# Kernel optimization log

Hardware: AMD Instinct MI355X
Metric: run time of the kernel (lower is better)

The kernel has to match this reference:

```python
import jax, jax.numpy as jnp
import numpy as np

H = 6      # n_attention_heads
BLK = 64


def adder1x1(x2d, w):
    """AdderNet 1x1 'convolution': Y[co, n] = -sum_ci |x2d[ci, n] - w[co, ci]|.
    Processed in output-channel blocks to bound the abs-diff intermediate.
    x2d: [Ci, N], w: [Co, Ci] -> [Co, N]
    """
    co, ci = w.shape
    wb = w.reshape(co // BLK, BLK, ci)
    def f(wblk):  # wblk: [BLK, Ci] -> [BLK, N]
        return -jnp.sum(jnp.abs(x2d[None, :, :] - wblk[:, :, None]), axis=1)
    return jax.lax.map(f, wb).reshape(co, -1)


def layernorm_all(y, w, b, eps=1e-5):
    # nn.LayerNorm([E, B, S]) applied to [1, E, B, S]: normalize over ALL of E,B,S
    mu = jnp.mean(y)
    var = jnp.mean((y - mu) ** 2)
    return (y - mu) * jax.lax.rsqrt(var + eps) * w + b


def layernorm_last(y, w, b, eps=1e-5):
    mu = jnp.mean(y, axis=-1, keepdims=True)
    var = jnp.mean((y - mu) ** 2, axis=-1, keepdims=True)
    return (y - mu) * jax.lax.rsqrt(var + eps) * w + b


def setup_inputs() -> dict:
    key = jax.random.key(0)
    ks = jax.random.split(key, 14)
    B, S, E = 8, 197, 384
    inp = {
        "x": jax.random.normal(ks[0], (B, S, E), jnp.float32),
        "wq": jax.random.normal(ks[1], (E, E), jnp.float32) * 0.05,
        "wk": jax.random.normal(ks[2], (E, E), jnp.float32) * 0.05,
        "wv": jax.random.normal(ks[3], (E, E), jnp.float32) * 0.05,
        "qln_w": 1.0 + 0.02 * jax.random.normal(ks[4], (E, B, S), jnp.float32),
        "qln_b": 0.02 * jax.random.normal(ks[5], (E, B, S), jnp.float32),
        "kln_w": 1.0 + 0.02 * jax.random.normal(ks[6], (E, B, S), jnp.float32),
        "kln_b": 0.02 * jax.random.normal(ks[7], (E, B, S), jnp.float32),
        "vln_w": 1.0 + 0.02 * jax.random.normal(ks[8], (E, B, S), jnp.float32),
        "vln_b": 0.02 * jax.random.normal(ks[9], (E, B, S), jnp.float32),
        "oln_w": 1.0 + 0.02 * jax.random.normal(ks[10], (E,), jnp.float32),
        "oln_b": 0.02 * jax.random.normal(ks[11], (E,), jnp.float32),
        "fc_w": jax.random.normal(ks[12], (E, E), jnp.float32) * 0.05,
        "fc_b": 0.02 * jax.random.normal(ks[13], (E,), jnp.float32),
    }
    return inp


def reference(x, wq, wk, wv, qln_w, qln_b, kln_w, kln_b, vln_w, vln_b,
              oln_w, oln_b, fc_w, fc_b):
    B, S, E = x.shape
    D = E // H
    scale = (2.0 * D * (1.0 - 2.0 / np.pi)) ** (-0.5)

    # torch: x.reshape(1, E, B, S) on contiguous [B,S,E] is a flat-buffer reshape
    x2d = x.reshape(E, B * S)  # [Ci, N]

    def proj(w, lw, lb):
        y = adder1x1(x2d, w).reshape(E, B, S)          # adder2d 1x1, bias=False
        y = layernorm_all(y, lw, lb)                    # LN over [E,B,S]
        y = y.reshape(B, S, H, D)                       # flat reshape (as torch)
        y = jnp.swapaxes(y, 1, 2)                       # [B,H,S,D]
        return y.reshape(B * H, S, D)

    q = proj(wq, qln_w, qln_b)
    k = proj(wk, kln_w, kln_b)
    v = proj(wv, vln_w, vln_b)

    att = jnp.einsum('bsd,btd->bst', q, k) * scale      # [B*H, S, S]
    att = jax.nn.softmax(att, axis=-1) + jnp.eye(S, dtype=x.dtype)
    o = jnp.einsum('bst,btd->bsd', att, v)              # [B*H, S, D]

    o = jnp.swapaxes(o.reshape(B, H, S, D), 1, 2).reshape(B, S, E)
    o = layernorm_last(o, oln_w, oln_b)
    return o @ fc_w.T + fc_b
```

## Files before the change

### kernel.cpp

```cpp
#include <hip/hip_runtime.h>
#include <math.h>

#ifndef M_PI
#define M_PI 3.14159265358979323846
#endif

#define B_ 8
#define S_ 197
#define E_ 384
#define H_ 6
#define D_ 64
#define N_ (B_*S_)
#define EN ((size_t)E_*N_)
#define NBLK_RED 591

__global__ __launch_bounds__(256) void k_adder(
    const float* __restrict__ x,
    const float* __restrict__ wq, const float* __restrict__ wk,
    const float* __restrict__ wv,
    float* __restrict__ P)
{
  const int z = blockIdx.z;
  const int p = z >> 1, c = z & 1;
  const float* __restrict__ w = (p == 0) ? wq : (p == 1) ? wk : wv;
  const int co0 = blockIdx.x * 64;
  const int n0  = blockIdx.y * 32;
  const int cib = c * 192;

  __shared__ float Xs[16][32];
  __shared__ float Ws[16][64];

  const int tid = threadIdx.x;
  const int tx = tid & 15;
  const int ty = tid >> 4;

  const int xr = tid >> 4, xc = (tid & 15) * 2;
  const int wr = tid >> 2, wc = (tid & 3) * 4;

  const bool xok = (n0 + xc + 1) < N_;
  const float* xg = x + (size_t)(cib + xr) * N_ + n0 + xc;
  const float* wg = w + (size_t)(co0 + wr) * E_ + cib + wc;

  float2 xv = xok ? *(const float2*)xg : make_float2(0.f, 0.f);
  float4 wv4 = *(const float4*)wg;

  float acc[4][2];
  #pragma unroll
  for (int i = 0; i < 4; ++i) { acc[i][0] = 0.f; acc[i][1] = 0.f; }

  #pragma unroll 1
  for (int t = 0; t < 12; ++t) {
    if (t > 0) __syncthreads();
    *(float2*)(&Xs[xr][xc]) = xv;
    Ws[wc + 0][wr] = wv4.x; Ws[wc + 1][wr] = wv4.y;
    Ws[wc + 2][wr] = wv4.z; Ws[wc + 3][wr] = wv4.w;
    __syncthreads();
    if (t < 11) {
      xg += (size_t)16 * N_;
      wg += 16;
      xv = xok ? *(const float2*)xg : make_float2(0.f, 0.f);
      wv4 = *(const float4*)wg;
    }
    #pragma unroll
    for (int cc = 0; cc < 16; ++cc) {
      float2 x2 = *(const float2*)(&Xs[cc][tx * 2]);
      float4 w4 = *(const float4*)(&Ws[cc][ty * 4]);
      float xa[2] = {x2.x, x2.y};
      float wa[4] = {w4.x, w4.y, w4.z, w4.w};
      #pragma unroll
      for (int i = 0; i < 4; ++i)
        #pragma unroll
        for (int j = 0; j < 2; ++j)
          acc[i][j] += fabsf(xa[j] - wa[i]);
    }
  }

  const int nb = n0 + tx * 2;
  if (nb + 1 < N_) {
    #pragma unroll
    for (int i = 0; i < 4; ++i) {
      int co = co0 + ty * 4 + i;
      float2 yv; yv.x = acc[i][0]; yv.y = acc[i][1];
      *(float2*)(P + (size_t)z * EN + (size_t)co * N_ + nb) = yv;
    }
  }
}

__global__ __launch_bounds__(256) void k_reduceY(
    float* __restrict__ wsbuf, float* __restrict__ partials)
{
  const int p = blockIdx.y;
  float* P0 = wsbuf + (size_t)(2 * p) * EN;
  const float* P1 = wsbuf + (size_t)(2 * p + 1) * EN;
  const int tid = threadIdx.x;
  size_t i = ((size_t)blockIdx.x * 256 + tid) * 4;
  float4 a = *(const float4*)(P0 + i);
  float4 b = *(const float4*)(P1 + i);
  float4 y;
  y.x = -(a.x + b.x); y.y = -(a.y + b.y);
  y.z = -(a.z + b.z); y.w = -(a.w + b.w);
  *(float4*)(P0 + i) = y;
  float s1 = y.x + y.y + y.z + y.w;
  float s2 = y.x * y.x + y.y * y.y + y.z * y.z + y.w * y.w;
  #pragma unroll
  for (int off = 32; off > 0; off >>= 1) {
    s1 += __shfl_down(s1, off);
    s2 += __shfl_down(s2, off);
  }
  __shared__ float red[8];
  int wid = tid >> 6, lane = tid & 63;
  if (lane == 0) { red[wid * 2] = s1; red[wid * 2 + 1] = s2; }
  __syncthreads();
  if (tid == 0) {
    float t1 = red[0] + red[2] + red[4] + red[6];
    float t2 = red[1] + red[3] + red[5] + red[7];
    partials[((size_t)p * NBLK_RED + blockIdx.x) * 2 + 0] = t1;
    partials[((size_t)p * NBLK_RED + blockIdx.x) * 2 + 1] = t2;
  }
}

__global__ __launch_bounds__(256) void k_stats(
    const float* __restrict__ partials, float* __restrict__ stats)
{
  const int p = blockIdx.x;
  const int tid = threadIdx.x;
  float s1 = 0.f, s2 = 0.f;
  for (int i = tid; i < NBLK_RED; i += 256) {
    s1 += partials[((size_t)p * NBLK_RED + i) * 2 + 0];
    s2 += partials[((size_t)p * NBLK_RED + i) * 2 + 1];
  }
  #pragma unroll
  for (int off = 32; off > 0; off >>= 1) {
    s1 += __shfl_down(s1, off);
    s2 += __shfl_down(s2, off);
  }
  __shared__ float red[8];
  int wid = tid >> 6, lane = tid & 63;
  if (lane == 0) { red[wid * 2] = s1; red[wid * 2 + 1] = s2; }
  __syncthreads();
  if (tid == 0) {
    float S1 = red[0] + red[2] + red[4] + red[6];
    float S2 = red[1] + red[3] + red[5] + red[7];
    float mean = S1 / (float)EN;
    float var = S2 / (float)EN - mean * mean;
    stats[p * 2 + 0] = mean;
    stats[p * 2 + 1] = rsqrtf(var + 1e-5f);
  }
}

__global__ __launch_bounds__(256) void k_lnall(
    float* __restrict__ wsbuf, const float* __restrict__ stats,
    const float* __restrict__ w0, const float* __restrict__ b0,
    const float* __restrict__ w1, const float* __restrict__ b1,
    const float* __restrict__ w2, const float* __restrict__ b2)
{
  const int p = blockIdx.y;
  const float* __restrict__ w = (p == 0) ? w0 : (p == 1) ? w1 : w2;
  const float* __restrict__ b = (p == 0) ? b0 : (p == 1) ? b1 : b2;
  const float mean = stats[p * 2 + 0];
  const float rstd = stats[p * 2 + 1];
  size_t i = ((size_t)blockIdx.x * 256 + threadIdx.x) * 4;
  const float* Yp = wsbuf + (size_t)(2 * p) * EN;
  float* Zp = wsbuf + (size_t)(2 * p + 1) * EN;
  float4 y = *(const float4*)(Yp + i);
  float4 wv = *(const float4*)(w + i);
  float4 bv = *(const float4*)(b + i);
  float4 z;
  z.x = (y.x - mean) * rstd * wv.x + bv.x;
  z.y = (y.y - mean) * rstd * wv.y + bv.y;
  z.z = (y.z - mean) * rstd * wv.z + bv.z;
  z.w = (y.w - mean) * rstd * wv.w + bv.w;
  *(float4*)(Zp + i) = z;
}

__global__ __launch_bounds__(256) void k_attn(
    const float* __restrict__ zq, const float* __restrict__ zk,
    const float* __restrict__ zv, float* __restrict__ obuf, float scale)
{
  const int bh = blockIdx.x, b = bh / H_, h = bh % H_;
  const int s0 = blockIdx.y * 32;

  __shared__ float Qs[64][36];
  __shared__ float KVs[64][68];
  __shared__ float Ps[32][200];
  __shared__ float linv[32];

  const int tid = threadIdx.x;
  const int tx = tid & 15, ty = tid >> 4;

  #pragma unroll
  for (int it = 0; it < 2; ++it) {
    int idx = tid + it * 256;
    int sl = idx >> 4, c4 = (idx & 15) * 4;
    int s = s0 + sl;
    float4 v = make_float4(0.f, 0.f, 0.f, 0.f);
    if (s < S_) v = *(const float4*)(zq + (size_t)(b * S_ + s) * E_ + h * D_ + c4);
    Qs[c4 + 0][sl] = v.x; Qs[c4 + 1][sl] = v.y;
    Qs[c4 + 2][sl] = v.z; Qs[c4 + 3][sl] = v.w;
  }

  float accS[4][2][4];
  #pragma unroll
  for (int tt = 0; tt < 4; ++tt)
    #pragma unroll
    for (int r = 0; r < 2; ++r)
      #pragma unroll
      for (int j = 0; j < 4; ++j) accS[tt][r][j] = 0.f;

  #pragma unroll
  for (int tt = 0; tt < 4; ++tt) {
    __syncthreads();
    #pragma unroll
    for (int it = 0; it < 4; ++it) {
      int idx = tid + it * 256;
      int tl = idx >> 4, c4 = (idx & 15) * 4;
      int t = tt * 64 + tl;
      float4 u = make_float4(0.f, 0.f, 0.f, 0.f);
      if (t < S_) u = *(const float4*)(zk + (size_t)(b * S_ + t) * E_ + h * D_ + c4);
      KVs[c4 + 0][tl] = u.x; KVs[c4 + 1][tl] = u.y;
      KVs[c4 + 2][tl] = u.z; KVs[c4 + 3][tl] = u.w;
    }
    __syncthreads();
    #pragma unroll 8
    for (int d = 0; d < 64; ++d) {
      float2 q2 = *(const float2*)(&Qs[d][2 * ty]);
      float4 k4 = *(const float4*)(&KVs[d][tx * 4]);
      float ka[4] = {k4.x, k4.y, k4.z, k4.w};
      #pragma unroll
      for (int j = 0; j < 4; ++j) {
        accS[tt][0][j] += q2.x * ka[j];
        accS[tt][1][j] += q2.y * ka[j];
      }
    }
  }

  float mr0 = -1e30f, mr1 = -1e30f;
  #pragma unroll
  for (int tt = 0; tt < 4; ++tt)
    #pragma unroll
    for (int j = 0; j < 4; ++j) {
      int t = tt * 64 + tx * 4 + j;
      float v0 = (t < S_) ? accS[tt][0][j] * scale : -1e30f;
      float v1 = (t < S_) ? accS[tt][1][j] * scale : -1e30f;
      accS[tt][0][j] = v0; accS[tt][1][j] = v1;
      mr0 = fmaxf(mr0, v0); mr1 = fmaxf(mr1, v1);
    }
  #pragma unroll
  for (int off = 1; off < 16; off <<= 1) {
    mr0 = fmaxf(mr0, __shfl_xor(mr0, off));
    mr1 = fmaxf(mr1, __shfl_xor(mr1, off));
  }
  float sr0 = 0.f, sr1 = 0.f;
  #pragma unroll
  for (int tt = 0; tt < 4; ++tt)
    #pragma unroll
    for (int j = 0; j < 4; ++j) {
      float p0 = __expf(accS[tt][0][j] - mr0);
      float p1 = __expf(accS[tt][1][j] - mr1);
      accS[tt][0][j] = p0; accS[tt][1][j] = p1;
      sr0 += p0; sr1 += p1;
    }
  #pragma unroll
  for (int off = 1; off < 16; off <<= 1) {
    sr0 += __shfl_xor(sr0, off);
    sr1 += __shfl_xor(sr1, off);
  }
  if (tx == 0) { linv[2 * ty] = 1.f / sr0; linv[2 * ty + 1] = 1.f / sr1; }
  #pragma unroll
  for (int tt = 0; tt < 4; ++tt) {
    int t4 = tt * 64 + tx * 4;
    if (t4 < 200) {
      *(float4*)(&Ps[2 * ty][t4]) =
          make_float4(accS[tt][0][0], accS[tt][0][1], accS[tt][0][2], accS[tt][0][3]);
      *(float4*)(&Ps[2 * ty + 1][t4]) =
          make_float4(accS[tt][1][0], accS[tt][1][1], accS[tt][1][2], accS[tt][1][3]);
    }
  }

  float accO[2][4];
  #pragma unroll
  for (int r = 0; r < 2; ++r)
    #pragma unroll
    for (int j = 0; j < 4; ++j) accO[r][j] = 0.f;

  #pragma unroll
  for (int tt = 0; tt < 4; ++tt) {
    __syncthreads();
    #pragma unroll
    for (int it = 0; it < 4; ++it) {
      int idx = tid + it * 256;
      int tl = idx >> 4, c4 = (idx & 15) * 4;
      int t = tt * 64 + tl;
      float4 u = make_float4(0.f, 0.f, 0.f, 0.f);
      if (t < S_) u = *(const float4*)(zv + (size_t)(b * S_ + t) * E_ + h * D_ + c4);
      *(float4*)(&KVs[tl][c4]) = u;
    }
    __syncthreads();
    const int tmax = (tt < 3) ? 64 : 8;
    #pragma unroll 8
    for (int tl = 0; tl < tmax; ++tl) {
      float p0 = Ps[2 * ty][tt * 64 + tl];
      float p1 = Ps[2 * ty + 1][tt * 64 + tl];
      float4 v4 = *(const float4*)(&KVs[tl][tx * 4]);
      float va[4] = {v4.x, v4.y, v4.z, v4.w};
      #pragma unroll
      for (int j = 0; j < 4; ++j) {
        accO[0][j] += p0 * va[j];
        accO[1][j] += p1 * va[j];
      }
    }
  }

  #pragma unroll
  for (int r = 0; r < 2; ++r) {
    int s = s0 + 2 * ty + r;
    if (s < S_) {
      float inv = linv[2 * ty + r];
      float4 vs = *(const float4*)(zv + (size_t)(b * S_ + s) * E_ + h * D_ + tx * 4);
      float4 o;
      o.x = accO[r][0] * inv + vs.x;
      o.y = accO[r][1] * inv + vs.y;
      o.z = accO[r][2] * inv + vs.z;
      o.w = accO[r][3] * inv + vs.w;
      *(float4*)(obuf + (size_t)(b * S_ + s) * E_ + h * D_ + tx * 4) = o;
    }
  }
}

__global__ __launch_bounds__(256) void k_lnlast(
    const float* __restrict__ obuf,
    const float* __restrict__ lw, const float* __restrict__ lb,
    float* __restrict__ oln)
{
  const int row = blockIdx.x * 4 + (threadIdx.x >> 6);
  const int lane = threadIdx.x & 63;
  const float* base = obuf + (size_t)row * E_;
  float v[6];
  float s1 = 0.f;
  #pragma unroll
  for (int j = 0; j < 6; ++j) { v[j] = base[lane + 64 * j]; s1 += v[j]; }
  #pragma unroll
  for (int off = 32; off > 0; off >>= 1) s1 += __shfl_xor(s1, off);
  float mean = s1 * (1.f / E_);
  float s2 = 0.f;
  #pragma unroll
  for (int j = 0; j < 6; ++j) { float d = v[j] - mean; s2 += d * d; }
  #pragma unroll
  for (int off = 32; off > 0; off >>= 1) s2 += __shfl_xor(s2, off);
  float rstd = rsqrtf(s2 * (1.f / E_) + 1e-5f);
  float* ob = oln + (size_t)row * E_;
  #pragma unroll
  for (int j = 0; j < 6; ++j) {
    int e = lane + 64 * j;
    ob[e] = (v[j] - mean) * rstd * lw[e] + lb[e];
  }
}

__global__ __launch_bounds__(256) void k_fc(
    const float* __restrict__ oln, const float* __restrict__ fcw,
    const float* __restrict__ fcb, float* __restrict__ out)
{
  const int j0 = blockIdx.x * 64, n0 = blockIdx.y * 64;
  __shared__ float Xs[16][64];
  __shared__ float Ws[16][64];
  const int tid = threadIdx.x;
  const int tx = tid & 15, ty = tid >> 4;
  float acc[4][4];
  #pragma unroll
  for (int i = 0; i < 4; ++i)
    #pragma unroll
    for (int j = 0; j < 4; ++j) acc[i][j] = 0.f;

  for (int e0 = 0; e0 < E_; e0 += 16) {
    {
      int nl = tid >> 2, c4 = (tid & 3) * 4;
      int n = n0 + nl;
      float4 v = make_float4(0.f, 0.f, 0.f, 0.f);
      if (n < N_) v = *(const float4*)(oln + (size_t)n * E_ + e0 + c4);
      Xs[c4 + 0][nl] = v.x; Xs[c4 + 1][nl] = v.y;
      Xs[c4 + 2][nl] = v.z; Xs[c4 + 3][nl] = v.w;
      float4 u = *(const float4*)(fcw + (size_t)(j0 + nl) * E_ + e0 + c4);
      Ws[c4 + 0][nl] = u.x; Ws[c4 + 1][nl] = u.y;
      Ws[c4 + 2][nl] = u.z; Ws[c4 + 3][nl] = u.w;
    }
    __syncthreads();
    #pragma unroll
    for (int cc = 0; cc < 16; ++cc) {
      float4 xv = *(const float4*)(&Xs[cc][tx * 4]);
      float4 wv4 = *(const float4*)(&Ws[cc][ty * 4]);
      float xa[4] = {xv.x, xv.y, xv.z, xv.w};
      float wa[4] = {wv4.x, wv4.y, wv4.z, wv4.w};
      #pragma unroll
      for (int i = 0; i < 4; ++i)
        #pragma unroll
        for (int j = 0; j < 4; ++j)
          acc[i][j] += wa[i] * xa[j];
    }
    __syncthreads();
  }
  #pragma unroll
  for (int jj = 0; jj < 4; ++jj) {
    int n = n0 + tx * 4 + jj;
    if (n < N_) {
      int jc = j0 + ty * 4;
      float4 o;
      o.x = acc[0][jj] + fcb[jc + 0];
      o.y = acc[1][jj] + fcb[jc + 1];
      o.z = acc[2][jj] + fcb[jc + 2];
      o.w = acc[3][jj] + fcb[jc + 3];
      *(float4*)(out + (size_t)n * E_ + jc) = o;
    }
  }
}

extern "C" void kernel_launch(void* const* d_in, const int* in_sizes, int n_in,
                              void* d_out, int out_size, void* d_ws, size_t ws_size,
                              hipStream_t stream)
{
  const float* x   = (const float*)d_in[0];
  const float* wq  = (const float*)d_in[1];
  const float* wk  = (const float*)d_in[2];
  const float* wv  = (const float*)d_in[3];
  const float* qw  = (const float*)d_in[4];
  const float* qb  = (const float*)d_in[5];
  const float* kw  = (const float*)d_in[6];
  const float* kb  = (const float*)d_in[7];
  const float* vw  = (const float*)d_in[8];
  const float* vb  = (const float*)d_in[9];
  const float* ow  = (const float*)d_in[10];
  const float* obp = (const float*)d_in[11];
  const float* fcw = (const float*)d_in[12];
  const float* fcb = (const float*)d_in[13];
  float* out = (float*)d_out;
  float* ws  = (float*)d_ws;

  float* obuf  = ws + 6 * EN;
  float* oln   = ws + 7 * EN;
  float* part  = ws + 8 * EN;
  float* stats = part + 3 * NBLK_RED * 2;

  const float scale = (float)pow(2.0 * D_ * (1.0 - 2.0 / M_PI), -0.5);

  k_adder<<<dim3(6, 50, 6), 256, 0, stream>>>(x, wq, wk, wv, ws);
  k_reduceY<<<dim3(NBLK_RED, 3), 256, 0, stream>>>(ws, part);
  k_stats<<<dim3(3), 256, 0, stream>>>(part, stats);
  k_lnall<<<dim3(NBLK_RED, 3), 256, 0, stream>>>(ws, stats, qw, qb, kw, kb, vw, vb);
  const float* zq = ws + 1 * EN;
  const float* zk = ws + 3 * EN;
  const float* zv = ws + 5 * EN;
  k_attn<<<dim3(48, 7), 256, 0, stream>>>(zq, zk, zv, obuf, scale);
  k_lnlast<<<dim3(394), 256, 0, stream>>>(obuf, ow, obp, oln);
  k_fc<<<dim3(6, 25), 256, 0, stream>>>(oln, fcw, fcb, out);
}
```

Baseline: 114.6 us.

## Retile adder, attention and FC kernels with 4-way Ci split and shuffle softmax

The adder projection now uses 64x64 output tiles with a 4x4 register block, double-buffered shared memory, and a 4-way split over input channels. The reduce kernel sums four partials instead of two, and the workspace layout is adjusted to match. The attention kernel processes 16 query rows per block, keeps probabilities in registers and broadcasts them with wave shuffles instead of staging them in shared memory. The FC kernel moves to smaller 32-row tiles to launch more blocks. The aim is more parallelism and better register reuse, at the cost of extra partial-buffer traffic and recomputed K/V loads per block.

```diff
diff --git a/kernel.cpp b/kernel.cpp
--- a/kernel.cpp
+++ b/kernel.cpp
@@ -21,67 +21,68 @@
     float* __restrict__ P)
 {
   const int z = blockIdx.z;
-  const int p = z >> 1, c = z & 1;
+  const int p = z >> 2, c = z & 3;
   const float* __restrict__ w = (p == 0) ? wq : (p == 1) ? wk : wv;
   const int co0 = blockIdx.x * 64;
-  const int n0  = blockIdx.y * 32;
-  const int cib = c * 192;
-
-  __shared__ float Xs[16][32];
-  __shared__ float Ws[16][64];
+  const int n0  = blockIdx.y * 64;
+  const int cib = c * 96;
+
+  __shared__ float Xs[2][16][68];
+  __shared__ float Ws[2][16][68];
 
   const int tid = threadIdx.x;
   const int tx = tid & 15;
   const int ty = tid >> 4;
 
-  const int xr = tid >> 4, xc = (tid & 15) * 2;
+  const int xr = tid >> 4, xc = (tid & 15) * 4;
   const int wr = tid >> 2, wc = (tid & 3) * 4;
 
-  const bool xok = (n0 + xc + 1) < N_;
+  const bool xok = (n0 + xc + 3) < N_;
   const float* xg = x + (size_t)(cib + xr) * N_ + n0 + xc;
   const float* wg = w + (size_t)(co0 + wr) * E_ + cib + wc;
 
-  float2 xv = xok ? *(const float2*)xg : make_float2(0.f, 0.f);
+  float4 xv = xok ? *(const float4*)xg : make_float4(0.f, 0.f, 0.f, 0.f);
   float4 wv4 = *(const float4*)wg;
 
-  float acc[4][2];
-  #pragma unroll
-  for (int i = 0; i < 4; ++i) { acc[i][0] = 0.f; acc[i][1] = 0.f; }
+  float acc[4][4];
+  #pragma unroll
+  for (int i = 0; i < 4; ++i)
+    #pragma unroll
+    for (int j = 0; j < 4; ++j) acc[i][j] = 0.f;
 
   #pragma unroll 1
-  for (int t = 0; t < 12; ++t) {
-    if (t > 0) __syncthreads();
-    *(float2*)(&Xs[xr][xc]) = xv;
-    Ws[wc + 0][wr] = wv4.x; Ws[wc + 1][wr] = wv4.y;
-    Ws[wc + 2][wr] = wv4.z; Ws[wc + 3][wr] = wv4.w;
-    __syncthreads();
-    if (t < 11) {
+  for (int t = 0; t < 6; ++t) {
+    const int buf = t & 1;
+    *(float4*)(&Xs[buf][xr][xc]) = xv;
+    Ws[buf][wc + 0][wr] = wv4.x; Ws[buf][wc + 1][wr] = wv4.y;
+    Ws[buf][wc + 2][wr] = wv4.z; Ws[buf][wc + 3][wr] = wv4.w;
+    __syncthreads();
+    if (t < 5) {
       xg += (size_t)16 * N_;
       wg += 16;
-      xv = xok ? *(const float2*)xg : make_float2(0.f, 0.f);
+      xv = xok ? *(const float4*)xg : make_float4(0.f, 0.f, 0.f, 0.f);
       wv4 = *(const float4*)wg;
     }
     #pragma unroll
     for (int cc = 0; cc < 16; ++cc) {
-      float2 x2 = *(const float2*)(&Xs[cc][tx * 2]);
-      float4 w4 = *(const float4*)(&Ws[cc][ty * 4]);
-      float xa[2] = {x2.x, x2.y};
-      float wa[4] = {w4.x, w4.y, w4.z, w4.w};
+      float4 a = *(const float4*)(&Xs[buf][cc][tx * 4]);
+      float4 b = *(const float4*)(&Ws[buf][cc][ty * 4]);
+      float xa[4] = {a.x, a.y, a.z, a.w};
+      float wa[4] = {b.x, b.y, b.z, b.w};
       #pragma unroll
       for (int i = 0; i < 4; ++i)
         #pragma unroll
-        for (int j = 0; j < 2; ++j)
+        for (int j = 0; j < 4; ++j)
           acc[i][j] += fabsf(xa[j] - wa[i]);
     }
   }
 
-  const int nb = n0 + tx * 2;
-  if (nb + 1 < N_) {
+  if ((n0 + tx * 4 + 3) < N_) {
     #pragma unroll
     for (int i = 0; i < 4; ++i) {
       int co = co0 + ty * 4 + i;
-      float2 yv; yv.x = acc[i][0]; yv.y = acc[i][1];
-      *(float2*)(P + (size_t)z * EN + (size_t)co * N_ + nb) = yv;
+      float4 yv = make_float4(acc[i][0], acc[i][1], acc[i][2], acc[i][3]);
+      *(float4*)(P + (size_t)z * EN + (size_t)co * N_ + n0 + tx * 4) = yv;
     }
   }
 }
@@ -90,15 +91,18 @@
     float* __restrict__ wsbuf, float* __restrict__ partials)
 {
   const int p = blockIdx.y;
-  float* P0 = wsbuf + (size_t)(2 * p) * EN;
-  const float* P1 = wsbuf + (size_t)(2 * p + 1) * EN;
+  float* P0 = wsbuf + (size_t)(4 * p) * EN;
   const int tid = threadIdx.x;
   size_t i = ((size_t)blockIdx.x * 256 + tid) * 4;
   float4 a = *(const float4*)(P0 + i);
-  float4 b = *(const float4*)(P1 + i);
+  float4 b = *(const float4*)(P0 + EN + i);
+  float4 cc = *(const float4*)(P0 + 2 * EN + i);
+  float4 d = *(const float4*)(P0 + 3 * EN + i);
   float4 y;
-  y.x = -(a.x + b.x); y.y = -(a.y + b.y);
-  y.z = -(a.z + b.z); y.w = -(a.w + b.w);
+  y.x = -(a.x + b.x + cc.x + d.x);
+  y.y = -(a.y + b.y + cc.y + d.y);
+  y.z = -(a.z + b.z + cc.z + d.z);
+  y.w = -(a.w + b.w + cc.w + d.w);
   *(float4*)(P0 + i) = y;
   float s1 = y.x + y.y + y.z + y.w;
   float s2 = y.x * y.x + y.y * y.y + y.z * y.z + y.w * y.w;
@@ -160,17 +164,17 @@
   const float mean = stats[p * 2 + 0];
   const float rstd = stats[p * 2 + 1];
   size_t i = ((size_t)blockIdx.x * 256 + threadIdx.x) * 4;
-  const float* Yp = wsbuf + (size_t)(2 * p) * EN;
-  float* Zp = wsbuf + (size_t)(2 * p + 1) * EN;
+  const float* Yp = wsbuf + (size_t)(4 * p) * EN;
+  float* Zp = wsbuf + (size_t)(4 * p + 1) * EN;
   float4 y = *(const float4*)(Yp + i);
   float4 wv = *(const float4*)(w + i);
   float4 bv = *(const float4*)(b + i);
-  float4 z;
-  z.x = (y.x - mean) * rstd * wv.x + bv.x;
-  z.y = (y.y - mean) * rstd * wv.y + bv.y;
-  z.z = (y.z - mean) * rstd * wv.z + bv.z;
-  z.w = (y.w - mean) * rstd * wv.w + bv.w;
-  *(float4*)(Zp + i) = z;
+  float4 zv;
+  zv.x = (y.x - mean) * rstd * wv.x + bv.x;
+  zv.y = (y.y - mean) * rstd * wv.y + bv.y;
+  zv.z = (y.z - mean) * rstd * wv.z + bv.z;
+  zv.w = (y.w - mean) * rstd * wv.w + bv.w;
+  *(float4*)(Zp + i) = zv;
 }
 
 __global__ __launch_bounds__(256) void k_attn(
@@ -178,34 +182,28 @@
     const float* __restrict__ zv, float* __restrict__ obuf, float scale)
 {
   const int bh = blockIdx.x, b = bh / H_, h = bh % H_;
-  const int s0 = blockIdx.y * 32;
-
-  __shared__ float Qs[64][36];
+  const int s0 = blockIdx.y * 16;
+
+  __shared__ float Qs[16][68];
   __shared__ float KVs[64][68];
-  __shared__ float Ps[32][200];
-  __shared__ float linv[32];
 
   const int tid = threadIdx.x;
-  const int tx = tid & 15, ty = tid >> 4;
-
-  #pragma unroll
-  for (int it = 0; it < 2; ++it) {
-    int idx = tid + it * 256;
-    int sl = idx >> 4, c4 = (idx & 15) * 4;
+  const int tx = tid & 15;
+  const int ty = tid >> 4;
+
+  {
+    int sl = tid >> 4, c4 = (tid & 15) * 4;
     int s = s0 + sl;
     float4 v = make_float4(0.f, 0.f, 0.f, 0.f);
     if (s < S_) v = *(const float4*)(zq + (size_t)(b * S_ + s) * E_ + h * D_ + c4);
-    Qs[c4 + 0][sl] = v.x; Qs[c4 + 1][sl] = v.y;
-    Qs[c4 + 2][sl] = v.z; Qs[c4 + 3][sl] = v.w;
-  }
-
-  float accS[4][2][4];
+    *(float4*)(&Qs[sl][c4]) = v;
+  }
+
+  float accS[4][4];
   #pragma unroll
   for (int tt = 0; tt < 4; ++tt)
     #pragma unroll
-    for (int r = 0; r < 2; ++r)
-      #pragma unroll
-      for (int j = 0; j < 4; ++j) accS[tt][r][j] = 0.f;
+    for (int j = 0; j < 4; ++j) accS[tt][j] = 0.f;
 
   #pragma unroll
   for (int tt = 0; tt < 4; ++tt) {
@@ -221,68 +219,47 @@
       KVs[c4 + 2][tl] = u.z; KVs[c4 + 3][tl] = u.w;
     }
     __syncthreads();
-    #pragma unroll 8
-    for (int d = 0; d < 64; ++d) {
-      float2 q2 = *(const float2*)(&Qs[d][2 * ty]);
-      float4 k4 = *(const float4*)(&KVs[d][tx * 4]);
-      float ka[4] = {k4.x, k4.y, k4.z, k4.w};
+    #pragma unroll
+    for (int dd = 0; dd < 16; ++dd) {
+      float4 q4 = *(const float4*)(&Qs[ty][dd * 4]);
+      float qa[4] = {q4.x, q4.y, q4.z, q4.w};
       #pragma unroll
-      for (int j = 0; j < 4; ++j) {
-        accS[tt][0][j] += q2.x * ka[j];
-        accS[tt][1][j] += q2.y * ka[j];
+      for (int k = 0; k < 4; ++k) {
+        float4 k4 = *(const float4*)(&KVs[dd * 4 + k][tx * 4]);
+        accS[tt][0] += qa[k] * k4.x;
+        accS[tt][1] += qa[k] * k4.y;
+        accS[tt][2] += qa[k] * k4.z;
+        accS[tt][3] += qa[k] * k4.w;
       }
     }
   }
 
-  float mr0 = -1e30f, mr1 = -1e30f;
+  float m = -1e30f;
   #pragma unroll
   for (int tt = 0; tt < 4; ++tt)
     #pragma unroll
     for (int j = 0; j < 4; ++j) {
       int t = tt * 64 + tx * 4 + j;
-      float v0 = (t < S_) ? accS[tt][0][j] * scale : -1e30f;
-      float v1 = (t < S_) ? accS[tt][1][j] * scale : -1e30f;
-      accS[tt][0][j] = v0; accS[tt][1][j] = v1;
-      mr0 = fmaxf(mr0, v0); mr1 = fmaxf(mr1, v1);
-    }
-  #pragma unroll
-  for (int off = 1; off < 16; off <<= 1) {
-    mr0 = fmaxf(mr0, __shfl_xor(mr0, off));
-    mr1 = fmaxf(mr1, __shfl_xor(mr1, off));
-  }
-  float sr0 = 0.f, sr1 = 0.f;
+      float v = (t < S_) ? accS[tt][j] * scale : -1e30f;
+      accS[tt][j] = v;
+      m = fmaxf(m, v);
+    }
+  #pragma unroll
+  for (int off = 1; off < 16; off <<= 1) m = fmaxf(m, __shfl_xor(m, off, 16));
+  float sum = 0.f;
   #pragma unroll
   for (int tt = 0; tt < 4; ++tt)
     #pragma unroll
     for (int j = 0; j < 4; ++j) {
-      float p0 = __expf(accS[tt][0][j] - mr0);
-      float p1 = __expf(accS[tt][1][j] - mr1);
-      accS[tt][0][j] = p0; accS[tt][1][j] = p1;
-      sr0 += p0; sr1 += p1;
-    }
-  #pragma unroll
-  for (int off = 1; off < 16; off <<= 1) {
-    sr0 += __shfl_xor(sr0, off);
-    sr1 += __shfl_xor(sr1, off);
-  }
-  if (tx == 0) { linv[2 * ty] = 1.f / sr0; linv[2 * ty + 1] = 1.f / sr1; }
-  #pragma unroll
-  for (int tt = 0; tt < 4; ++tt) {
-    int t4 = tt * 64 + tx * 4;
-    if (t4 < 200) {
-      *(float4*)(&Ps[2 * ty][t4]) =
-          make_float4(accS[tt][0][0], accS[tt][0][1], accS[tt][0][2], accS[tt][0][3]);
-      *(float4*)(&Ps[2 * ty + 1][t4]) =
-          make_float4(accS[tt][1][0], accS[tt][1][1], accS[tt][1][2], accS[tt][1][3]);
-    }
-  }
-
-  float accO[2][4];
-  #pragma unroll
-  for (int r = 0; r < 2; ++r)
-    #pragma unroll
-    for (int j = 0; j < 4; ++j) accO[r][j] = 0.f;
-
+      float pv = __expf(accS[tt][j] - m);
+      accS[tt][j] = pv;
+      sum += pv;
+    }
+  #pragma unroll
+  for (int off = 1; off < 16; off <<= 1) sum += __shfl_xor(sum, off, 16);
+  const float inv = 1.f / sum;
+
+  float accO[4] = {0.f, 0.f, 0.f, 0.f};
   #pragma unroll
   for (int tt = 0; tt < 4; ++tt) {
     __syncthreads();
@@ -296,34 +273,26 @@
       *(float4*)(&KVs[tl][c4]) = u;
     }
     __syncthreads();
-    const int tmax = (tt < 3) ? 64 : 8;
     #pragma unroll 8
-    for (int tl = 0; tl < tmax; ++tl) {
-      float p0 = Ps[2 * ty][tt * 64 + tl];
-      float p1 = Ps[2 * ty + 1][tt * 64 + tl];
+    for (int tl = 0; tl < 64; ++tl) {
+      float pp = __shfl(accS[tt][tl & 3], ((ty & 3) << 4) | (tl >> 2), 64);
       float4 v4 = *(const float4*)(&KVs[tl][tx * 4]);
-      float va[4] = {v4.x, v4.y, v4.z, v4.w};
-      #pragma unroll
-      for (int j = 0; j < 4; ++j) {
-        accO[0][j] += p0 * va[j];
-        accO[1][j] += p1 * va[j];
-      }
-    }
-  }
-
-  #pragma unroll
-  for (int r = 0; r < 2; ++r) {
-    int s = s0 + 2 * ty + r;
-    if (s < S_) {
-      float inv = linv[2 * ty + r];
-      float4 vs = *(const float4*)(zv + (size_t)(b * S_ + s) * E_ + h * D_ + tx * 4);
-      float4 o;
-      o.x = accO[r][0] * inv + vs.x;
-      o.y = accO[r][1] * inv + vs.y;
-      o.z = accO[r][2] * inv + vs.z;
-      o.w = accO[r][3] * inv + vs.w;
-      *(float4*)(obuf + (size_t)(b * S_ + s) * E_ + h * D_ + tx * 4) = o;
-    }
+      accO[0] += pp * v4.x;
+      accO[1] += pp * v4.y;
+      accO[2] += pp * v4.z;
+      accO[3] += pp * v4.w;
+    }
+  }
+
+  const int s = s0 + ty;
+  if (s < S_) {
+    float4 vs = *(const float4*)(zv + (size_t)(b * S_ + s) * E_ + h * D_ + tx * 4);
+    float4 o;
+    o.x = accO[0] * inv + vs.x;
+    o.y = accO[1] * inv + vs.y;
+    o.z = accO[2] * inv + vs.z;
+    o.w = accO[3] * inv + vs.w;
+    *(float4*)(obuf + (size_t)(b * S_ + s) * E_ + h * D_ + tx * 4) = o;
   }
 }
 
@@ -360,54 +329,53 @@
     const float* __restrict__ oln, const float* __restrict__ fcw,
     const float* __restrict__ fcb, float* __restrict__ out)
 {
-  const int j0 = blockIdx.x * 64, n0 = blockIdx.y * 64;
-  __shared__ float Xs[16][64];
-  __shared__ float Ws[16][64];
+  const int j0 = blockIdx.x * 64, n0 = blockIdx.y * 32;
+  __shared__ float Xs[16][36];
+  __shared__ float Ws[16][68];
   const int tid = threadIdx.x;
   const int tx = tid & 15, ty = tid >> 4;
-  float acc[4][4];
-  #pragma unroll
-  for (int i = 0; i < 4; ++i)
-    #pragma unroll
-    for (int j = 0; j < 4; ++j) acc[i][j] = 0.f;
+  float acc[4][2];
+  #pragma unroll
+  for (int i = 0; i < 4; ++i) { acc[i][0] = 0.f; acc[i][1] = 0.f; }
 
   for (int e0 = 0; e0 < E_; e0 += 16) {
     {
-      int nl = tid >> 2, c4 = (tid & 3) * 4;
+      int nl = tid >> 3, e2 = (tid & 7) * 2;
       int n = n0 + nl;
-      float4 v = make_float4(0.f, 0.f, 0.f, 0.f);
-      if (n < N_) v = *(const float4*)(oln + (size_t)n * E_ + e0 + c4);
-      Xs[c4 + 0][nl] = v.x; Xs[c4 + 1][nl] = v.y;
-      Xs[c4 + 2][nl] = v.z; Xs[c4 + 3][nl] = v.w;
-      float4 u = *(const float4*)(fcw + (size_t)(j0 + nl) * E_ + e0 + c4);
-      Ws[c4 + 0][nl] = u.x; Ws[c4 + 1][nl] = u.y;
-      Ws[c4 + 2][nl] = u.z; Ws[c4 + 3][nl] = u.w;
+      float2 v = make_float2(0.f, 0.f);
+      if (n < N_) v = *(const float2*)(oln + (size_t)n * E_ + e0 + e2);
+      Xs[e2 + 0][nl] = v.x; Xs[e2 + 1][nl] = v.y;
+      int jl = tid >> 2, c4 = (tid & 3) * 4;
+      float4 u = *(const float4*)(fcw + (size_t)(j0 + jl) * E_ + e0 + c4);
+      Ws[c4 + 0][jl] = u.x; Ws[c4 + 1][jl] = u.y;
+      Ws[c4 + 2][jl] = u.z; Ws[c4 + 3][jl] = u.w;
     }
     __syncthreads();
     #pragma unroll
     for (int cc = 0; cc < 16; ++cc) {
-      float4 xv = *(const float4*)(&Xs[cc][tx * 4]);
-      float4 wv4 = *(const float4*)(&Ws[cc][ty * 4]);
-      float xa[4] = {xv.x, xv.y, xv.z, xv.w};
-      float wa[4] = {wv4.x, wv4.y, wv4.z, wv4.w};
+      float2 x2 = *(const float2*)(&Xs[cc][tx * 2]);
+      float4 w4 = *(const float4*)(&Ws[cc][ty * 4]);
+      float xa[2] = {x2.x, x2.y};
+      float wa[4] = {w4.x, w4.y, w4.z, w4.w};
       #pragma unroll
-      for (int i = 0; i < 4; ++i)
-        #pragma unroll
-        for (int j = 0; j < 4; ++j)
-          acc[i][j] += wa[i] * xa[j];
-    }
-    __syncthreads();
-  }
-  #pragma unroll
-  for (int jj = 0; jj < 4; ++jj) {
-    int n = n0 + tx * 4 + jj;
+      for (int i = 0; i < 4; ++i) {
+        acc[i][0] += wa[i] * xa[0];
+        acc[i][1] += wa[i] * xa[1];
+      }
+    }
+    __syncthreads();
+  }
+  const int jc = j0 + ty * 4;
+  float4 bv = *(const float4*)(fcb + jc);
+  #pragma unroll
+  for (int jn = 0; jn < 2; ++jn) {
+    int n = n0 + tx * 2 + jn;
     if (n < N_) {
-      int jc = j0 + ty * 4;
       float4 o;
-      o.x = acc[0][jj] + fcb[jc + 0];
-      o.y = acc[1][jj] + fcb[jc + 1];
-      o.z = acc[2][jj] + fcb[jc + 2];
-      o.w = acc[3][jj] + fcb[jc + 3];
+      o.x = acc[0][jn] + bv.x;
+      o.y = acc[1][jn] + bv.y;
+      o.z = acc[2][jn] + bv.z;
+      o.w = acc[3][jn] + bv.w;
       *(float4*)(out + (size_t)n * E_ + jc) = o;
     }
   }
@@ -434,21 +402,21 @@
   float* out = (float*)d_out;
   float* ws  = (float*)d_ws;
 
-  float* obuf  = ws + 6 * EN;
-  float* oln   = ws + 7 * EN;
-  float* part  = ws + 8 * EN;
+  float* obuf  = ws + 0 * EN;
+  float* oln   = ws + 2 * EN;
+  float* part  = ws + 12 * EN;
   float* stats = part + 3 * NBLK_RED * 2;
 
   const float scale = (float)pow(2.0 * D_ * (1.0 - 2.0 / M_PI), -0.5);
 
-  k_adder<<<dim3(6, 50, 6), 256, 0, stream>>>(x, wq, wk, wv, ws);
+  k_adder<<<dim3(6, 25, 12), 256, 0, stream>>>(x, wq, wk, wv, ws);
   k_reduceY<<<dim3(NBLK_RED, 3), 256, 0, stream>>>(ws, part);
   k_stats<<<dim3(3), 256, 0, stream>>>(part, stats);
   k_lnall<<<dim3(NBLK_RED, 3), 256, 0, stream>>>(ws, stats, qw, qb, kw, kb, vw, vb);
   const float* zq = ws + 1 * EN;
-  const float* zk = ws + 3 * EN;
-  const float* zv = ws + 5 * EN;
-  k_attn<<<dim3(48, 7), 256, 0, stream>>>(zq, zk, zv, obuf, scale);
+  const float* zk = ws + 5 * EN;
+  const float* zv = ws + 9 * EN;
+  k_attn<<<dim3(48, 13), 256, 0, stream>>>(zq, zk, zv, obuf, scale);
   k_lnlast<<<dim3(394), 256, 0, stream>>>(obuf, ow, obp, oln);
-  k_fc<<<dim3(6, 25), 256, 0, stream>>>(oln, fcw, fcb, out);
-}
+  k_fc<<<dim3(6, 50), 256, 0, stream>>>(oln, fcw, fcb, out);
+}
```

Measured after the change: 269.0 us. +134.8%, slower.
